# Optimization experiments

Hardware: AMD Instinct MI355X
Metric: run time of the kernel (lower is better)

Reference implementation:

```python
import jax, jax.numpy as jnp
import numpy as np

WINDOW = 7
NUM_NODES = 20000
IN_CH = 8
HID = 64
N_TOTAL = WINDOW * NUM_NODES          # 140000 supra-nodes (window x nodes)
N_EDGES = N_TOTAL * 16                # avg degree 16
EPS = 1e-5                            # BatchNorm1d eps


def setup_inputs() -> dict:
    key = jax.random.key(0)
    ks = jax.random.split(key, 12)
    return {
        "_x": jax.random.normal(ks[0], (N_TOTAL, IN_CH), jnp.float32),
        "edge_idx": jax.random.randint(ks[1], (2, N_EDGES), 0, N_TOTAL, dtype=jnp.int32),
        "edge_wgt": jax.random.uniform(ks[2], (N_EDGES,), jnp.float32),
        # GCNConv 1 / 2 (weight stored as [in, out])
        "W1": jax.random.normal(ks[3], (IN_CH, HID), jnp.float32) / np.sqrt(IN_CH).astype(np.float32),
        "b1": jnp.zeros((HID,), jnp.float32),
        "W2": jax.random.normal(ks[4], (HID, HID), jnp.float32) / np.sqrt(HID).astype(np.float32),
        "b2": jnp.zeros((HID,), jnp.float32),
        # BatchNorm1d 1 / 2
        "gamma1": jnp.ones((HID,), jnp.float32),
        "beta1": jnp.zeros((HID,), jnp.float32),
        "gamma2": jnp.ones((HID,), jnp.float32),
        "beta2": jnp.zeros((HID,), jnp.float32),
        # LSTM 1: input 2*HID -> HID ; LSTM 2: HID -> HID (PyTorch gate order i,f,g,o)
        "Wih1": jax.random.normal(ks[5], (4 * HID, 2 * HID), jnp.float32) / np.sqrt(2 * HID).astype(np.float32),
        "Whh1": jax.random.normal(ks[6], (4 * HID, HID), jnp.float32) / np.sqrt(HID).astype(np.float32),
        "bih1": jnp.zeros((4 * HID,), jnp.float32),
        "bhh1": jnp.zeros((4 * HID,), jnp.float32),
        "Wih2": jax.random.normal(ks[7], (4 * HID, HID), jnp.float32) / np.sqrt(HID).astype(np.float32),
        "Whh2": jax.random.normal(ks[8], (4 * HID, HID), jnp.float32) / np.sqrt(HID).astype(np.float32),
        "bih2": jnp.zeros((4 * HID,), jnp.float32),
        "bhh2": jnp.zeros((4 * HID,), jnp.float32),
    }


def _batch_norm(x, gamma, beta):
    # training-mode BatchNorm1d: batch statistics, biased variance
    m = x.mean(axis=0)
    v = ((x - m) ** 2).mean(axis=0)
    return (x - m) * jax.lax.rsqrt(v + EPS) * gamma + beta


def _lstm(seq, Wih, Whh, bih, bhh):
    # seq: [T, B, D]; PyTorch gate order (i, f, g, o); zero initial state
    B = seq.shape[1]
    H = Whh.shape[1]
    h0 = jnp.zeros((B, H), seq.dtype)

    def step(carry, xt):
        h, c = carry
        gates = xt @ Wih.T + h @ Whh.T + bih + bhh   # [B, 4H]
        i, f, g, o = jnp.split(gates, 4, axis=1)
        c = jax.nn.sigmoid(f) * c + jax.nn.sigmoid(i) * jnp.tanh(g)
        h = jax.nn.sigmoid(o) * jnp.tanh(c)
        return (h, c), h

    (hT, _), ys = jax.lax.scan(step, (h0, h0), seq)
    return ys, hT


def _forward(_x, edge_idx, edge_wgt, W1, b1, W2, b2, gamma1, beta1, gamma2, beta2,
             Wih1, Whh1, bih1, bhh1, Wih2, Whh2, bih2, bhh2):
    # --- skip connection S: [num_nodes, in_ch + window - 1] ---
    S = _x.reshape(-1, WINDOW, NUM_NODES, IN_CH).transpose(0, 2, 1, 3).reshape(-1, WINDOW, IN_CH)
    S = jnp.concatenate([S[:, 0, :], S[:, 1:, IN_CH - 1]], axis=1)

    # --- symmetric GCN normalization with self loops (gcn_norm, fill=1.0) ---
    loop = jnp.arange(N_TOTAL, dtype=edge_idx.dtype)
    src = jnp.concatenate([edge_idx[0], loop])
    dst = jnp.concatenate([edge_idx[1], loop])
    w = jnp.concatenate([edge_wgt, jnp.ones((N_TOTAL,), edge_wgt.dtype)])
    deg = jax.ops.segment_sum(w, dst, num_segments=N_TOTAL)
    dinv = jnp.where(deg > 0, jax.lax.rsqrt(jnp.where(deg > 0, deg, 1.0)), 0.0)
    norm = dinv[src] * w * dinv[dst]  # [E+N]

    def gconv(h, W, b):
        msg = (h @ W)[src] * norm[:, None]                     # gather + scale
        return jax.ops.segment_sum(msg, dst, num_segments=N_TOTAL) + b  # scatter-add

    # dropout is identity in eval mode (deterministic baseline)
    X1 = _batch_norm(jax.nn.relu(gconv(_x, W1, b1)), gamma1, beta1)
    X2 = _batch_norm(jax.nn.relu(gconv(X1, W2, b2)), gamma2, beta2)

    Xc = jnp.concatenate([X1, X2], axis=1)                     # [window*nodes, 2H]
    Xc = Xc.reshape(-1, WINDOW, NUM_NODES, 2 * HID).transpose(1, 0, 2, 3)
    Xc = Xc.reshape(WINDOW, -1, 2 * HID)                       # [T, B*nodes, 2H]

    ys1, H1 = _lstm(Xc, Wih1, Whh1, bih1, bhh1)
    _, H2 = _lstm(ys1, Wih2, Whh2, bih2, bhh2)

    return jnp.concatenate([H1, H2, S], axis=1)  # [nodes, 2H + in_ch + window - 1]


def reference(_x, edge_idx, edge_wgt, W1, b1, W2, b2, gamma1, beta1, gamma2, beta2,
              Wih1, Whh1, bih1, bhh1, Wih2, Whh2, bih2, bhh2):
    return _forward(_x, edge_idx, edge_wgt, W1, b1, W2, b2, gamma1, beta1, gamma2, beta2,
                    Wih1, Whh1, bih1, bhh1, Wih2, Whh2, bih2, bhh2)
```

## Files before the change

### kernel.cpp

```cpp
#include <hip/hip_runtime.h>


#define N_TOT 140000
#define NQUAD 35000
#define NE    2240000
#define NODES 20000
#define TWIN  7
#define CIN   8
#define HD    64
#define OUTC  142
#define SLOTS 48
#define WQ    16383.0f
#define NTILES 1250
#define HTILES 8750

typedef __attribute__((ext_vector_type(8))) short short8;
typedef __attribute__((ext_vector_type(4))) float f32x4;

static __device__ __forceinline__ float fast_exp2(float x) {
  return __builtin_amdgcn_exp2f(x);
}
static __device__ __forceinline__ float fast_rcp(float x) {
  return __builtin_amdgcn_rcpf(x);
}
static __device__ __forceinline__ float sigf(float x) {
  return fast_rcp(1.0f + fast_exp2(-1.4426950408889634f * x));
}
static __device__ __forceinline__ float tanhf_(float x) {
  return 1.0f - 2.0f * fast_rcp(1.0f + fast_exp2(2.8853900817779268f * x));
}
static __device__ __forceinline__ ushort f2bf(float x) {
  union { float f; uint32_t u; } c; c.f = x;
  uint32_t r = c.u + 0x7fff + ((c.u >> 16) & 1);
  return (ushort)(r >> 16);
}
static __device__ __forceinline__ float bf2f(ushort h) {
  union { uint32_t u; float f; } c; c.u = ((uint32_t)h) << 16; return c.f;
}
static __device__ __forceinline__ float wdec(uint v) {
  return (float)(v & 16383u) * (1.0f / WQ);
}

__global__ __launch_bounds__(256) void k_wpack0(const float* __restrict__ Whh1,
                                                const float* __restrict__ Wih2,
                                                const float* __restrict__ Whh2,
                                                const float* __restrict__ bih2,
                                                const float* __restrict__ bhh2,
                                                ushort* __restrict__ Wphh1,
                                                ushort* __restrict__ Wpih2,
                                                ushort* __restrict__ Wphh2,
                                                float* __restrict__ bsum2) {
  int b = blockIdx.x;
  if (b < 192) {
    int which = b >> 6;
    int idx = (b & 63) * 256 + threadIdx.x;
    const float* W = (which == 0) ? Whh1 : (which == 1) ? Wih2 : Whh2;
    ushort* Wp = (which == 0) ? Wphh1 : (which == 1) ? Wpih2 : Wphh2;
    int j = idx & 7, lane = (idx >> 3) & 63, nt = (idx >> 9) & 15, kc = idx >> 13;
    int g = nt * 16 + (lane & 15);
    int k = kc * 32 + ((lane >> 4) << 3) + j;
    Wp[idx] = f2bf(W[g * 64 + k]);
  } else {
    bsum2[threadIdx.x] = bih2[threadIdx.x] + bhh2[threadIdx.x];
  }
}

__global__ __launch_bounds__(256) void k_mid1(const float* __restrict__ W2,
                                              const float* __restrict__ scale1,
                                              const float* __restrict__ shift1,
                                              ushort* __restrict__ Wp2,
                                              float* __restrict__ c2b) {
  int b = blockIdx.x;
  if (b < 16) {
    int idx = b * 256 + threadIdx.x;
    int jj = idx & 7, lane = (idx >> 3) & 63, nt = (idx >> 9) & 3, kc = idx >> 11;
    int j = nt * 16 + (lane & 15);
    int k = kc * 32 + ((lane >> 4) << 3) + jj;
    Wp2[idx] = f2bf(scale1[k] * W2[k * 64 + j]);
  } else if (threadIdx.x < HD) {
    int j = threadIdx.x;
    float s = 0.f;
    for (int k = 0; k < HD; ++k) s += shift1[k] * W2[k * 64 + j];
    c2b[j] = s;
  }
}

__global__ __launch_bounds__(256) void k_mid2(const float* __restrict__ Wih1,
                                              const float* __restrict__ scale1,
                                              const float* __restrict__ scale2,
                                              const float* __restrict__ shift1,
                                              const float* __restrict__ shift2,
                                              const float* __restrict__ bih1,
                                              const float* __restrict__ bhh1,
                                              ushort* __restrict__ Wp1,
                                              float* __restrict__ biasL1) {
  int b = blockIdx.x;
  if (b < 128) {
    int idx = b * 256 + threadIdx.x;
    int j = idx & 7, lane = (idx >> 3) & 63, nt = (idx >> 9) & 15, kc = idx >> 13;
    int g = nt * 16 + (lane & 15);
    int k = kc * 32 + ((lane >> 4) << 3) + j;
    float s = (k < HD) ? scale1[k] : scale2[k - HD];
    Wp1[idx] = f2bf(Wih1[g * 128 + k] * s);
  } else {
    int col = threadIdx.x;
    float s = bih1[col] + bhh1[col];
    for (int k = 0; k < HD; ++k) s += Wih1[col * 128 + k] * shift1[k];
    for (int k = 0; k < HD; ++k) s += Wih1[col * 128 + HD + k] * shift2[k];
    biasL1[col] = s;
  }
}

__global__ __launch_bounds__(256) void k_fill_direct(const int* __restrict__ srcI,
                                                     const int* __restrict__ dstI,
                                                     const float* __restrict__ w,
                                                     int* cursor,
                                                     uint* __restrict__ csr) {
  int e = blockIdx.x * 256 + threadIdx.x;
  if (e < NE) {
    int s = srcI[e], d = dstI[e];
    int pos = atomicAdd(&cursor[d], 1);
    if (pos < SLOTS) {
      uint q = (uint)(w[e] * WQ + 0.5f);
      csr[(size_t)d * SLOTS + pos] = ((uint)s << 14) | q;
    }
  }
}

__global__ __launch_bounds__(256) void k_prep4(const int* __restrict__ cursor,
                                               uint* __restrict__ csr,
                                               const float* __restrict__ x,
                                               float* __restrict__ dinv,
                                               ushort* __restrict__ xs) {
  int wv = (blockIdx.x * 256 + threadIdx.x) >> 6;
  int lane = threadIdx.x & 63;
  int nw = (gridDim.x * 256) >> 6;
  for (int p = wv; p < NQUAD; p += nw) {
    int d0 = p * 4;
    int len[4];
    float ws[4];
    #pragma unroll
    for (int r = 0; r < 4; ++r) {
      len[r] = min(cursor[d0 + r], SLOTS);
      ws[r] = (lane < len[r]) ? wdec(csr[(size_t)(d0 + r) * SLOTS + lane]) : 0.f;
    }
    #pragma unroll
    for (int m = 1; m < 64; m <<= 1) {
      #pragma unroll
      for (int r = 0; r < 4; ++r) ws[r] += __shfl_xor(ws[r], m);
    }
    float di[4];
    #pragma unroll
    for (int r = 0; r < 4; ++r) di[r] = rsqrtf(1.0f + ws[r]);
    if (lane < 4) dinv[d0 + lane] = di[lane];
    int lenM = (max(max(len[0], len[1]), max(len[2], len[3])) + 7) & ~7;
    #pragma unroll
    for (int r = 0; r < 4; ++r)
      if (lane >= len[r] && lane < lenM) csr[(size_t)(d0 + r) * SLOTS + lane] = 0u;
    if (lane < 4 * CIN) {
      int r = lane >> 3, c = lane & 7;
      xs[(size_t)(d0 + r) * CIN + c] = f2bf(di[r] * x[(size_t)(d0 + r) * CIN + c]);
    }
  }
}

__global__ __launch_bounds__(256) void k_gcn1(const ushort* __restrict__ xs,
                                              const float* __restrict__ dinv,
                                              const int* __restrict__ cursor,
                                              const uint* __restrict__ csr,
                                              const float* __restrict__ W1,
                                              const float* __restrict__ b1,
                                              ushort* __restrict__ A1,
                                              float* gsum, float* gsq) {
  __shared__ float w1s[CIN * HD];
  __shared__ float b1s[HD];
  for (int i = threadIdx.x; i < CIN * HD; i += 256) w1s[i] = W1[i];
  if (threadIdx.x < HD) b1s[threadIdx.x] = b1[threadIdx.x];
  __syncthreads();
  int wv = (blockIdx.x * 256 + threadIdx.x) >> 6;
  int lane = threadIdx.x & 63;
  int nw = (gridDim.x * 256) >> 6;
  int e8 = lane >> 3, c8 = lane & 7;
  float s = 0.f, q = 0.f;
  for (int p = wv; p < N_TOT / 2; p += nw) {
    int dA = p * 2, dB = dA + 1;
    const uint* rowA = csr + (size_t)dA * SLOTS;
    const uint* rowB = csr + (size_t)dB * SLOTS;
    int lenA = min(cursor[dA], SLOTS), lenB = min(cursor[dB], SLOTS);
    int lenM = (max(lenA, lenB) + 7) & ~7;
    float pA = 0.f, pB = 0.f;
    #pragma unroll 2
    for (int i = e8; i < lenM; i += 8) {
      uint ca = rowA[i];
      uint cb = rowB[i];
      pA += wdec(ca) * bf2f(xs[(size_t)(ca >> 14) * CIN + c8]);
      pB += wdec(cb) * bf2f(xs[(size_t)(cb >> 14) * CIN + c8]);
    }
    pA += __shfl_xor(pA, 8);  pB += __shfl_xor(pB, 8);
    pA += __shfl_xor(pA, 16); pB += __shfl_xor(pB, 16);
    pA += __shfl_xor(pA, 32); pB += __shfl_xor(pB, 32);
    pA += bf2f(xs[(size_t)dA * CIN + c8]);
    pB += bf2f(xs[(size_t)dB * CIN + c8]);
    float diA = dinv[dA], diB = dinv[dB];
    float accA = b1s[lane], accB = b1s[lane];
    #pragma unroll
    for (int c = 0; c < CIN; ++c) {
      float w = w1s[c * HD + lane];
      accA += diA * __shfl(pA, c) * w;
      accB += diB * __shfl(pB, c) * w;
    }
    float rA = fmaxf(accA, 0.f), rB = fmaxf(accB, 0.f);
    A1[(size_t)dA * HD + lane] = f2bf(rA);
    A1[(size_t)dB * HD + lane] = f2bf(rB);
    s += rA + rB; q += rA * rA + rB * rB;
  }
  atomicAdd(&gsum[lane], s);
  atomicAdd(&gsq[lane], q);
}

__global__ __launch_bounds__(64) void k_bnfin(const float* __restrict__ gsum,
                                              const float* __restrict__ gsq,
                                              const float* __restrict__ gamma,
                                              const float* __restrict__ beta,
                                              float* __restrict__ scale,
                                              float* __restrict__ shift) {
  int j = threadIdx.x;
  if (j < HD) {
    float m = gsum[j] / (float)N_TOT;
    float v = gsq[j] / (float)N_TOT - m * m;
    float sc = gamma[j] * rsqrtf(v + 1e-5f);
    scale[j] = sc;
    shift[j] = beta[j] - m * sc;
  }
}

__global__ __launch_bounds__(256) void k_gemm_h2(const ushort* __restrict__ A1,
                                                 const ushort* __restrict__ Wp2,
                                                 const float* __restrict__ c2b,
                                                 const float* __restrict__ dinv,
                                                 ushort* __restrict__ Hbs) {
  int t = threadIdx.x, wid = t >> 6, lane = t & 63;
  int tile = blockIdx.x * 4 + wid;
  if (tile >= HTILES) return;
  int g = lane >> 4, c = lane & 15;
  const ushort* ap = A1 + ((size_t)(tile * 16 + c)) * HD + g * 8;
  f32x4 acc[4];
  #pragma unroll
  for (int nt = 0; nt < 4; ++nt) {
    float bv = c2b[nt * 16 + c];
    acc[nt] = (f32x4){bv, bv, bv, bv};
  }
  #pragma unroll
  for (int kc = 0; kc < 2; ++kc) {
    short8 a = *reinterpret_cast<const short8*>(ap + kc * 32);
    #pragma unroll
    for (int nt = 0; nt < 4; ++nt) {
      short8 b = *reinterpret_cast<const short8*>(&Wp2[((kc * 4 + nt) * 64 + lane) * 8]);
      acc[nt] = __builtin_amdgcn_mfma_f32_16x16x32_bf16(a, b, acc[nt], 0, 0, 0);
    }
  }
  float dv[4];
  #pragma unroll
  for (int jr = 0; jr < 4; ++jr) dv[jr] = dinv[tile * 16 + g * 4 + jr];
  #pragma unroll
  for (int nt = 0; nt < 4; ++nt)
    #pragma unroll
    for (int jr = 0; jr < 4; ++jr) {
      int r = g * 4 + jr;
      Hbs[((size_t)(tile * 16 + r)) * HD + nt * 16 + c] = f2bf(dv[jr] * acc[nt][jr]);
    }
}

__global__ __launch_bounds__(256) void k_spmm2(const ushort* __restrict__ Hbs,
                                               const float* __restrict__ dinv,
                                               const int* __restrict__ cursor,
                                               const uint* __restrict__ csr,
                                               const float* __restrict__ bias,
                                               ushort* __restrict__ A2,
                                               float* gsum, float* gsq) {
  int wv = (blockIdx.x * 256 + threadIdx.x) >> 6;
  int lane = threadIdx.x & 63;
  int nw = (gridDim.x * 256) >> 6;
  float b = bias[lane];
  float s = 0.f, q = 0.f;
  for (int p = wv; p < NQUAD; p += nw) {
    int d0 = p * 4;
    const uint* row0 = csr + (size_t)(d0 + 0) * SLOTS;
    const uint* row1 = csr + (size_t)(d0 + 1) * SLOTS;
    const uint* row2 = csr + (size_t)(d0 + 2) * SLOTS;
    const uint* row3 = csr + (size_t)(d0 + 3) * SLOTS;
    int l0 = min(cursor[d0 + 0], SLOTS), l1 = min(cursor[d0 + 1], SLOTS);
    int l2 = min(cursor[d0 + 2], SLOTS), l3 = min(cursor[d0 + 3], SLOTS);
    int lenM = (max(max(l0, l1), max(l2, l3)) + 7) & ~7;
    float a0 = bf2f(Hbs[(size_t)(d0 + 0) * HD + lane]);
    float a1 = bf2f(Hbs[(size_t)(d0 + 1) * HD + lane]);
    float a2 = bf2f(Hbs[(size_t)(d0 + 2) * HD + lane]);
    float a3 = bf2f(Hbs[(size_t)(d0 + 3) * HD + lane]);
    for (int i0 = 0; i0 < lenM; i0 += 4) {
      uint cv0[4], cv1[4], cv2[4], cv3[4];
      #pragma unroll
      for (int j = 0; j < 4; ++j) {
        cv0[j] = row0[i0 + j]; cv1[j] = row1[i0 + j];
        cv2[j] = row2[i0 + j]; cv3[j] = row3[i0 + j];
      }
      ushort h0[4], h1[4], h2[4], h3[4];
      #pragma unroll
      for (int j = 0; j < 4; ++j) {
        h0[j] = Hbs[((size_t)(cv0[j] >> 14)) * HD + lane];
        h1[j] = Hbs[((size_t)(cv1[j] >> 14)) * HD + lane];
        h2[j] = Hbs[((size_t)(cv2[j] >> 14)) * HD + lane];
        h3[j] = Hbs[((size_t)(cv3[j] >> 14)) * HD + lane];
      }
      #pragma unroll
      for (int j = 0; j < 4; ++j) {
        a0 = fmaf(wdec(cv0[j]), bf2f(h0[j]), a0);
        a1 = fmaf(wdec(cv1[j]), bf2f(h1[j]), a1);
        a2 = fmaf(wdec(cv2[j]), bf2f(h2[j]), a2);
        a3 = fmaf(wdec(cv3[j]), bf2f(h3[j]), a3);
      }
    }
    float r0 = fmaxf(dinv[d0 + 0] * a0 + b, 0.f);
    float r1 = fmaxf(dinv[d0 + 1] * a1 + b, 0.f);
    float r2 = fmaxf(dinv[d0 + 2] * a2 + b, 0.f);
    float r3 = fmaxf(dinv[d0 + 3] * a3 + b, 0.f);
    A2[(size_t)(d0 + 0) * HD + lane] = f2bf(r0);
    A2[(size_t)(d0 + 1) * HD + lane] = f2bf(r1);
    A2[(size_t)(d0 + 2) * HD + lane] = f2bf(r2);
    A2[(size_t)(d0 + 3) * HD + lane] = f2bf(r3);
    s += r0 + r1 + r2 + r3;
    q += r0 * r0 + r1 * r1 + r2 * r2 + r3 * r3;
  }
  atomicAdd(&gsum[lane], s);
  atomicAdd(&gsq[lane], q);
}

__global__ __launch_bounds__(256) void k_lstm5(const ushort* __restrict__ A1,
                                               const ushort* __restrict__ A2,
                                               const ushort* __restrict__ Wp1,
                                               const ushort* __restrict__ Wphh1,
                                               const ushort* __restrict__ Wpih2,
                                               const ushort* __restrict__ Wphh2,
                                               const float* __restrict__ biasL1,
                                               const float* __restrict__ bsum2,
                                               const float* __restrict__ x,
                                               float* __restrict__ out) {
  __shared__ ushort h1s[2][1024];
  __shared__ ushort h2s[2][1024];
  int t = threadIdx.x;
  int q = t >> 6, lane = t & 63;
  int tile = blockIdx.x;
  int g = lane >> 4, c = lane & 15;

  float c1[4], c2[4];
  #pragma unroll
  for (int i = 0; i < 4; ++i) { c1[i] = 0.f; c2[i] = 0.f; }

  int hr[2];
  #pragma unroll
  for (int kc = 0; kc < 2; ++kc)
    hr[kc] = (c * 64 + kc * 32 + g * 8) ^ ((c & 7) << 3);
  int hw[4];
  #pragma unroll
  for (int jr = 0; jr < 4; ++jr) {
    int r = g * 4 + jr, j = q * 16 + c;
    hw[jr] = (r * 64 + j) ^ ((r & 7) << 3);
  }
  float bL1[4], bL2[4];
  #pragma unroll
  for (int gi = 0; gi < 4; ++gi) {
    bL1[gi] = biasL1[gi * 64 + q * 16 + c];
    bL2[gi] = bsum2[gi * 64 + q * 16 + c];
  }

  for (int step = 0; step < TWIN; ++step) {
    int pw = step & 1, pr = pw ^ 1;
    size_t nodeoff = (size_t)(step * NODES + tile * 16 + c) * HD + g * 8;
    const ushort* a1p = A1 + nodeoff;
    const ushort* a2p = A2 + nodeoff;

    f32x4 acc[4];
    #pragma unroll
    for (int gi = 0; gi < 4; ++gi) acc[gi] = (f32x4){bL1[gi], bL1[gi], bL1[gi], bL1[gi]};
    #pragma unroll
    for (int kc = 0; kc < 4; ++kc) {
      const ushort* ap = (kc < 2) ? (a1p + kc * 32) : (a2p + (kc - 2) * 32);
      short8 a = *reinterpret_cast<const short8*>(ap);
      #pragma unroll
      for (int gi = 0; gi < 4; ++gi) {
        short8 b = *reinterpret_cast<const short8*>(&Wp1[((kc * 16 + gi * 4 + q) * 64 + lane) * 8]);
        acc[gi] = __builtin_amdgcn_mfma_f32_16x16x32_bf16(a, b, acc[gi], 0, 0, 0);
      }
    }
    if (step > 0) {
      #pragma unroll
      for (int kc = 0; kc < 2; ++kc) {
        short8 a = *reinterpret_cast<const short8*>(&h1s[pr][hr[kc]]);
        #pragma unroll
        for (int gi = 0; gi < 4; ++gi) {
          short8 b = *reinterpret_cast<const short8*>(&Wphh1[((kc * 16 + gi * 4 + q) * 64 + lane) * 8]);
          acc[gi] = __builtin_amdgcn_mfma_f32_16x16x32_bf16(a, b, acc[gi], 0, 0, 0);
        }
      }
    }
    #pragma unroll
    for (int jr = 0; jr < 4; ++jr) {
      float gi_ = acc[0][jr], gf = acc[1][jr], gg = acc[2][jr], go = acc[3][jr];
      float cc = sigf(gf) * c1[jr] + sigf(gi_) * tanhf_(gg);
      c1[jr] = cc;
      float h = sigf(go) * tanhf_(cc);
      h1s[pw][hw[jr]] = f2bf(h);
      if (step == TWIN - 1) {
        int r = g * 4 + jr, j = q * 16 + c;
        out[(size_t)(tile * 16 + r) * OUTC + j] = h;
      }
    }
    __syncthreads();

    #pragma unroll
    for (int gi = 0; gi < 4; ++gi) acc[gi] = (f32x4){bL2[gi], bL2[gi], bL2[gi], bL2[gi]};
    #pragma unroll
    for (int kc = 0; kc < 2; ++kc) {
      short8 a = *reinterpret_cast<const short8*>(&h1s[pw][hr[kc]]);
      #pragma unroll
      for (int gi = 0; gi < 4; ++gi) {
        short8 b = *reinterpret_cast<const short8*>(&Wpih2[((kc * 16 + gi * 4 + q) * 64 + lane) * 8]);
        acc[gi] = __builtin_amdgcn_mfma_f32_16x16x32_bf16(a, b, acc[gi], 0, 0, 0);
      }
    }
    if (step > 0) {
      #pragma unroll
      for (int kc = 0; kc < 2; ++kc) {
        short8 a = *reinterpret_cast<const short8*>(&h2s[pr][hr[kc]]);
        #pragma unroll
        for (int gi = 0; gi < 4; ++gi) {
          short8 b = *reinterpret_cast<const short8*>(&Wphh2[((kc * 16 + gi * 4 + q) * 64 + lane) * 8]);
          acc[gi] = __builtin_amdgcn_mfma_f32_16x16x32_bf16(a, b, acc[gi], 0, 0, 0);
        }
      }
    }
    #pragma unroll
    for (int jr = 0; jr < 4; ++jr) {
      float gi_ = acc[0][jr], gf = acc[1][jr], gg = acc[2][jr], go = acc[3][jr];
      float cc = sigf(gf) * c2[jr] + sigf(gi_) * tanhf_(gg);
      c2[jr] = cc;
      float h = sigf(go) * tanhf_(cc);
      h2s[pw][hw[jr]] = f2bf(h);
      if (step == TWIN - 1) {
        int r = g * 4 + jr, j = q * 16 + c;
        out[(size_t)(tile * 16 + r) * OUTC + HD + j] = h;
      }
    }
    __syncthreads();
  }

  for (int idx = t; idx < 16 * 14; idx += 256) {
    int r = idx / 14, cc = idx - r * 14;
    int n = tile * 16 + r;
    float v = (cc < CIN) ? x[(size_t)n * CIN + cc]
                         : x[((size_t)(cc - (CIN - 1)) * NODES + n) * CIN + (CIN - 1)];
    out[(size_t)n * OUTC + 128 + cc] = v;
  }
}

extern "C" void kernel_launch(void* const* d_in, const int* in_sizes, int n_in,
                              void* d_out, int out_size, void* d_ws, size_t ws_size,
                              hipStream_t stream) {
  const float* x      = (const float*)d_in[0];
  const int*   ei     = (const int*)d_in[1];
  const float* ew     = (const float*)d_in[2];
  const float* W1     = (const float*)d_in[3];
  const float* b1     = (const float*)d_in[4];
  const float* W2     = (const float*)d_in[5];
  const float* b2     = (const float*)d_in[6];
  const float* gamma1 = (const float*)d_in[7];
  const float* beta1  = (const float*)d_in[8];
  const float* gamma2 = (const float*)d_in[9];
  const float* beta2  = (const float*)d_in[10];
  const float* Wih1   = (const float*)d_in[11];
  const float* Whh1   = (const float*)d_in[12];
  const float* bih1   = (const float*)d_in[13];
  const float* bhh1   = (const float*)d_in[14];
  const float* Wih2   = (const float*)d_in[15];
  const float* Whh2   = (const float*)d_in[16];
  const float* bih2   = (const float*)d_in[17];
  const float* bhh2   = (const float*)d_in[18];
  const int* srcI = ei;
  const int* dstI = ei + NE;
  float* out = (float*)d_out;

  char* base = (char*)d_ws;
  size_t off = 0;
  auto alloc = [&](size_t bytes) -> void* {
    void* p = base + off;
    off = (off + bytes + 255) & ~(size_t)255;
    return p;
  };
  float* dinv   = (float*)alloc(N_TOT * 4);
  ushort* xs    = (ushort*)alloc((size_t)N_TOT * CIN * 2);
  ushort* Wp1   = (ushort*)alloc(32768 * 2);
  ushort* Wphh1 = (ushort*)alloc(16384 * 2);
  ushort* Wpih2 = (ushort*)alloc(16384 * 2);
  ushort* Wphh2 = (ushort*)alloc(16384 * 2);
  ushort* Wp2   = (ushort*)alloc(4096 * 2);
  float* c2b    = (float*)alloc(HD * 4);
  float* biasL1 = (float*)alloc(256 * 4);
  float* bsum2  = (float*)alloc(256 * 4);
  float* scale1 = (float*)alloc(HD * 4);
  float* shift1 = (float*)alloc(HD * 4);
  float* scale2 = (float*)alloc(HD * 4);
  float* shift2 = (float*)alloc(HD * 4);
  char* zstart = base + off;
  int*   cursor = (int*)alloc(N_TOT * 4);
  float* sum1   = (float*)alloc(HD * 4);
  float* sq1    = (float*)alloc(HD * 4);
  float* sum2   = (float*)alloc(HD * 4);
  float* sq2    = (float*)alloc(HD * 4);
  size_t zbytes = (size_t)((base + off) - zstart);
  uint*   csr = (uint*)alloc((size_t)N_TOT * SLOTS * 4);
  ushort* Hbs = (ushort*)alloc((size_t)N_TOT * HD * 2);
  ushort* A1  = (ushort*)alloc((size_t)N_TOT * HD * 2);
  ushort* A2  = (ushort*)alloc((size_t)N_TOT * HD * 2);

  hipMemsetAsync(zstart, 0, zbytes, stream);
  k_wpack0<<<193, 256, 0, stream>>>(Whh1, Wih2, Whh2, bih2, bhh2,
                                    Wphh1, Wpih2, Wphh2, bsum2);
  k_fill_direct<<<(NE + 255) / 256, 256, 0, stream>>>(srcI, dstI, ew, cursor, csr);
  k_prep4<<<1024, 256, 0, stream>>>(cursor, csr, x, dinv, xs);
  k_gcn1<<<1024, 256, 0, stream>>>(xs, dinv, cursor, csr, W1, b1, A1, sum1, sq1);
  k_bnfin<<<1, 64, 0, stream>>>(sum1, sq1, gamma1, beta1, scale1, shift1);
  k_mid1<<<17, 256, 0, stream>>>(W2, scale1, shift1, Wp2, c2b);
  k_gemm_h2<<<(HTILES + 3) / 4, 256, 0, stream>>>(A1, Wp2, c2b, dinv, Hbs);
  k_spmm2<<<1024, 256, 0, stream>>>(Hbs, dinv, cursor, csr, b2, A2, sum2, sq2);
  k_bnfin<<<1, 64, 0, stream>>>(sum2, sq2, gamma2, beta2, scale2, shift2);
  k_mid2<<<129, 256, 0, stream>>>(Wih1, scale1, scale2, shift1, shift2,
                                  bih1, bhh1, Wp1, biasL1);
  k_lstm5<<<NTILES, 256, 0, stream>>>(A1, A2, Wp1, Wphh1, Wpih2, Wphh2,
                                      biasL1, bsum2, x, out);
}
```

Baseline: 602.3 us.

## Partition CSR fill by destination range and widen gcn1/spmm2 row batching

The edge-to-CSR fill kernel now has each block scan a chunk of edges but handle only destinations inside one of 8 node partitions. This is meant to localise atomics and scattered writes to a smaller slice of memory that fits in cache, at the cost of reading dstI 8 times. The first GCN layer now processes four destination rows per wave instead of two, and the second layer's SpMM unroll grows from 4 to 8 edges. Both aim for more memory-level parallelism on the gathers, with more register pressure in exchange.

```diff
diff --git a/kernel.cpp b/kernel.cpp
--- a/kernel.cpp
+++ b/kernel.cpp
@@ -11,6 +11,8 @@
 #define OUTC  142
 #define SLOTS 48
 #define WQ    16383.0f
+#define NPART 8
+#define PSIZE 17500
 #define NTILES 1250
 #define HTILES 8750
 
@@ -111,18 +113,30 @@
   }
 }
 
-__global__ __launch_bounds__(256) void k_fill_direct(const int* __restrict__ srcI,
-                                                     const int* __restrict__ dstI,
-                                                     const float* __restrict__ w,
-                                                     int* cursor,
-                                                     uint* __restrict__ csr) {
-  int e = blockIdx.x * 256 + threadIdx.x;
-  if (e < NE) {
-    int s = srcI[e], d = dstI[e];
-    int pos = atomicAdd(&cursor[d], 1);
-    if (pos < SLOTS) {
-      uint q = (uint)(w[e] * WQ + 0.5f);
-      csr[(size_t)d * SLOTS + pos] = ((uint)s << 14) | q;
+__global__ __launch_bounds__(256) void k_fill_part(const int* __restrict__ srcI,
+                                                   const int* __restrict__ dstI,
+                                                   const float* __restrict__ w,
+                                                   int* cursor,
+                                                   uint* __restrict__ csr) {
+  int b = blockIdx.x;
+  int part = b & (NPART - 1);
+  int chunk = b >> 3;
+  int nchunks = gridDim.x >> 3;
+  int per = (NE + nchunks - 1) / nchunks;
+  int lo = chunk * per;
+  int hi = min(lo + per, NE);
+  int plo = part * PSIZE;
+  for (int e = lo + threadIdx.x; e < hi; e += 256) {
+    int d = dstI[e];
+    unsigned du = (unsigned)(d - plo);
+    if (du < (unsigned)PSIZE) {
+      int s = srcI[e];
+      float wv = w[e];
+      int pos = atomicAdd(&cursor[d], 1);
+      if (pos < SLOTS) {
+        uint q = (uint)(wv * WQ + 0.5f);
+        csr[(size_t)d * SLOTS + pos] = ((uint)s << 14) | q;
+      }
     }
   }
 }
@@ -182,37 +196,52 @@
   int nw = (gridDim.x * 256) >> 6;
   int e8 = lane >> 3, c8 = lane & 7;
   float s = 0.f, q = 0.f;
-  for (int p = wv; p < N_TOT / 2; p += nw) {
-    int dA = p * 2, dB = dA + 1;
-    const uint* rowA = csr + (size_t)dA * SLOTS;
-    const uint* rowB = csr + (size_t)dB * SLOTS;
-    int lenA = min(cursor[dA], SLOTS), lenB = min(cursor[dB], SLOTS);
-    int lenM = (max(lenA, lenB) + 7) & ~7;
-    float pA = 0.f, pB = 0.f;
+  for (int p = wv; p < NQUAD; p += nw) {
+    int d0 = p * 4;
+    const uint* row0 = csr + (size_t)(d0 + 0) * SLOTS;
+    const uint* row1 = csr + (size_t)(d0 + 1) * SLOTS;
+    const uint* row2 = csr + (size_t)(d0 + 2) * SLOTS;
+    const uint* row3 = csr + (size_t)(d0 + 3) * SLOTS;
+    int l0 = min(cursor[d0 + 0], SLOTS), l1 = min(cursor[d0 + 1], SLOTS);
+    int l2 = min(cursor[d0 + 2], SLOTS), l3 = min(cursor[d0 + 3], SLOTS);
+    int lenM = (max(max(l0, l1), max(l2, l3)) + 7) & ~7;
+    float p0 = 0.f, p1 = 0.f, p2 = 0.f, p3 = 0.f;
     #pragma unroll 2
     for (int i = e8; i < lenM; i += 8) {
-      uint ca = rowA[i];
-      uint cb = rowB[i];
-      pA += wdec(ca) * bf2f(xs[(size_t)(ca >> 14) * CIN + c8]);
-      pB += wdec(cb) * bf2f(xs[(size_t)(cb >> 14) * CIN + c8]);
-    }
-    pA += __shfl_xor(pA, 8);  pB += __shfl_xor(pB, 8);
-    pA += __shfl_xor(pA, 16); pB += __shfl_xor(pB, 16);
-    pA += __shfl_xor(pA, 32); pB += __shfl_xor(pB, 32);
-    pA += bf2f(xs[(size_t)dA * CIN + c8]);
-    pB += bf2f(xs[(size_t)dB * CIN + c8]);
-    float diA = dinv[dA], diB = dinv[dB];
-    float accA = b1s[lane], accB = b1s[lane];
+      uint c0 = row0[i], c1 = row1[i], c2 = row2[i], c3 = row3[i];
+      p0 += wdec(c0) * bf2f(xs[(size_t)(c0 >> 14) * CIN + c8]);
+      p1 += wdec(c1) * bf2f(xs[(size_t)(c1 >> 14) * CIN + c8]);
+      p2 += wdec(c2) * bf2f(xs[(size_t)(c2 >> 14) * CIN + c8]);
+      p3 += wdec(c3) * bf2f(xs[(size_t)(c3 >> 14) * CIN + c8]);
+    }
+    #pragma unroll
+    for (int m = 8; m < 64; m <<= 1) {
+      p0 += __shfl_xor(p0, m); p1 += __shfl_xor(p1, m);
+      p2 += __shfl_xor(p2, m); p3 += __shfl_xor(p3, m);
+    }
+    p0 += bf2f(xs[(size_t)(d0 + 0) * CIN + c8]);
+    p1 += bf2f(xs[(size_t)(d0 + 1) * CIN + c8]);
+    p2 += bf2f(xs[(size_t)(d0 + 2) * CIN + c8]);
+    p3 += bf2f(xs[(size_t)(d0 + 3) * CIN + c8]);
+    float di0 = dinv[d0 + 0], di1 = dinv[d0 + 1];
+    float di2 = dinv[d0 + 2], di3 = dinv[d0 + 3];
+    float a0 = b1s[lane], a1 = b1s[lane], a2 = b1s[lane], a3 = b1s[lane];
     #pragma unroll
     for (int c = 0; c < CIN; ++c) {
-      float w = w1s[c * HD + lane];
-      accA += diA * __shfl(pA, c) * w;
-      accB += diB * __shfl(pB, c) * w;
-    }
-    float rA = fmaxf(accA, 0.f), rB = fmaxf(accB, 0.f);
-    A1[(size_t)dA * HD + lane] = f2bf(rA);
-    A1[(size_t)dB * HD + lane] = f2bf(rB);
-    s += rA + rB; q += rA * rA + rB * rB;
+      float wgt = w1s[c * HD + lane];
+      a0 += di0 * __shfl(p0, c) * wgt;
+      a1 += di1 * __shfl(p1, c) * wgt;
+      a2 += di2 * __shfl(p2, c) * wgt;
+      a3 += di3 * __shfl(p3, c) * wgt;
+    }
+    float r0 = fmaxf(a0, 0.f), r1 = fmaxf(a1, 0.f);
+    float r2 = fmaxf(a2, 0.f), r3 = fmaxf(a3, 0.f);
+    A1[(size_t)(d0 + 0) * HD + lane] = f2bf(r0);
+    A1[(size_t)(d0 + 1) * HD + lane] = f2bf(r1);
+    A1[(size_t)(d0 + 2) * HD + lane] = f2bf(r2);
+    A1[(size_t)(d0 + 3) * HD + lane] = f2bf(r3);
+    s += r0 + r1 + r2 + r3;
+    q += r0 * r0 + r1 * r1 + r2 * r2 + r3 * r3;
   }
   atomicAdd(&gsum[lane], s);
   atomicAdd(&gsq[lane], q);
@@ -296,23 +325,23 @@
     float a1 = bf2f(Hbs[(size_t)(d0 + 1) * HD + lane]);
     float a2 = bf2f(Hbs[(size_t)(d0 + 2) * HD + lane]);
     float a3 = bf2f(Hbs[(size_t)(d0 + 3) * HD + lane]);
-    for (int i0 = 0; i0 < lenM; i0 += 4) {
-      uint cv0[4], cv1[4], cv2[4], cv3[4];
-      #pragma unroll
-      for (int j = 0; j < 4; ++j) {
+    for (int i0 = 0; i0 < lenM; i0 += 8) {
+      uint cv0[8], cv1[8], cv2[8], cv3[8];
+      #pragma unroll
+      for (int j = 0; j < 8; ++j) {
         cv0[j] = row0[i0 + j]; cv1[j] = row1[i0 + j];
         cv2[j] = row2[i0 + j]; cv3[j] = row3[i0 + j];
       }
-      ushort h0[4], h1[4], h2[4], h3[4];
-      #pragma unroll
-      for (int j = 0; j < 4; ++j) {
+      ushort h0[8], h1[8], h2[8], h3[8];
+      #pragma unroll
+      for (int j = 0; j < 8; ++j) {
         h0[j] = Hbs[((size_t)(cv0[j] >> 14)) * HD + lane];
         h1[j] = Hbs[((size_t)(cv1[j] >> 14)) * HD + lane];
         h2[j] = Hbs[((size_t)(cv2[j] >> 14)) * HD + lane];
         h3[j] = Hbs[((size_t)(cv3[j] >> 14)) * HD + lane];
       }
       #pragma unroll
-      for (int j = 0; j < 4; ++j) {
+      for (int j = 0; j < 8; ++j) {
         a0 = fmaf(wdec(cv0[j]), bf2f(h0[j]), a0);
         a1 = fmaf(wdec(cv1[j]), bf2f(h1[j]), a1);
         a2 = fmaf(wdec(cv2[j]), bf2f(h2[j]), a2);
@@ -524,7 +553,7 @@
   hipMemsetAsync(zstart, 0, zbytes, stream);
   k_wpack0<<<193, 256, 0, stream>>>(Whh1, Wih2, Whh2, bih2, bhh2,
                                     Wphh1, Wpih2, Wphh2, bsum2);
-  k_fill_direct<<<(NE + 255) / 256, 256, 0, stream>>>(srcI, dstI, ew, cursor, csr);
+  k_fill_part<<<1024, 256, 0, stream>>>(srcI, dstI, ew, cursor, csr);
   k_prep4<<<1024, 256, 0, stream>>>(cursor, csr, x, dinv, xs);
   k_gcn1<<<1024, 256, 0, stream>>>(xs, dinv, cursor, csr, W1, b1, A1, sum1, sq1);
   k_bnfin<<<1, 64, 0, stream>>>(sum1, sq1, gamma1, beta1, scale1, shift1);
```

New measurement: 521.9 us. 13.3% less time.
